# Optimization experiments

Hardware: AMD Instinct MI355X
Metric: run time of the kernel (lower is better)

Reference implementation:

```python
import jax, jax.numpy as jnp
import numpy as np

N, E, EQ, DIM = 50000, 800000, 100000, 256


def setup_inputs() -> dict:
    key = jax.random.key(0)
    k1, k2, k3, k4, k5 = jax.random.split(key, 5)
    edges = jax.random.randint(k1, (2, EQ), 0, N)
    adj_row = jax.random.randint(k2, (E,), 0, N)
    adj_col = jax.random.randint(k3, (E,), 0, N)
    node_weight = jax.random.uniform(k4, (N,), dtype=jnp.float32)
    # torchhd-style bipolar hypervectors scaled by sqrt(1/dim)
    scale = (1.0 / DIM) ** 0.5
    node_vectors = jnp.sign(jax.random.normal(k5, (N, DIM), dtype=jnp.float32)) * scale
    return dict(edges=edges, adj_row=adj_row, adj_col=adj_col,
                node_weight=node_weight, node_vectors=node_vectors)


def reference(edges, adj_row, adj_col, node_weight, node_vectors):
    n = node_vectors.shape[0]
    # get_random_node_vectors: embedding * node_weight
    x = node_vectors * node_weight[:, None]                       # [N, dim]
    # one_hop_x = A @ x ; two_hop_x = A @ one_hop_x (binary adjacency)
    one_hop = jax.ops.segment_sum(x[adj_col], adj_row, num_segments=n)       # [N, dim]
    two_hop = jax.ops.segment_sum(one_hop[adj_col], adj_row, num_segments=n)  # [N, dim]
    deg = jax.ops.segment_sum(jnp.ones(adj_row.shape, x.dtype), adj_row, num_segments=n)  # [N]
    s, t = edges[0], edges[1]
    dot = lambda a, b: (a * b).sum(-1)
    count_1_1 = dot(one_hop[s], one_hop[t])
    count_1_2 = dot(one_hop[s], two_hop[t]) + dot(two_hop[s], one_hop[t])
    count_2_2 = dot(two_hop[s] - deg[s][:, None] * x[s],
                    two_hop[t] - deg[t][:, None] * x[t])
    count_self_1_2 = dot(one_hop[s], two_hop[s]) + dot(one_hop[t], two_hop[t])
    return (count_1_1, count_1_2, count_2_2, count_self_1_2)
```

## Files before the change

### kernel.cpp

```cpp
#include <hip/hip_runtime.h>

#define DIM 256
#define NODE_U2 192
#define NODE_U4 96
#define SLOT_OH_U2 64
#define SLOT_TH_U2 128
#define SLOT_OH_U4 32
#define SLOT_TH_U4 64

#define NSL 8

__device__ __forceinline__ unsigned int f2bf_rne(float f) {
    unsigned int u = __float_as_uint(f);
    return (u + 0x7fffu + ((u >> 16) & 1u)) >> 16;
}
__device__ __forceinline__ float bf_lo(unsigned int u) {
    return __uint_as_float(u << 16);
}
__device__ __forceinline__ float bf_hi(unsigned int u) {
    return __uint_as_float(u & 0xffff0000u);
}
__device__ __forceinline__ unsigned int pack2(float a, float b) {
    return f2bf_rne(a) | (f2bf_rne(b) << 16);
}

#define ACC8(v)                                            \
    do {                                                   \
        a0 += bf_lo((v).x); a1 += bf_hi((v).x);            \
        a2 += bf_lo((v).y); a3 += bf_hi((v).y);            \
        a4 += bf_lo((v).z); a5 += bf_hi((v).z);            \
        a6 += bf_lo((v).w); a7 += bf_hi((v).w);            \
    } while (0)

__global__ void x_and_hist_kernel(const float* __restrict__ nv,
                                  const float* __restrict__ w,
                                  uint2* __restrict__ cmb,
                                  uint2* __restrict__ xs_sl,
                                  int total_u2, int N,
                                  const int* __restrict__ adj_row,
                                  int* __restrict__ cnt, int E) {
    int i0 = blockIdx.x * blockDim.x + threadIdx.x;
    int stride = gridDim.x * blockDim.x;
    for (int i = i0; i < total_u2; i += stride) {
        float4 v = reinterpret_cast<const float4*>(nv)[i];
        int node = i >> 6;
        int j = i & 63;
        float wt = w[node];
        uint2 r;
        r.x = pack2(v.x * wt, v.y * wt);
        r.y = pack2(v.z * wt, v.w * wt);
        cmb[(size_t)node * NODE_U2 + j] = r;
        int s = j >> 3;
        xs_sl[((size_t)s * N + node) * 8 + (j & 7)] = r;
    }
    for (int e = i0; e < E; e += stride) {
        atomicAdd(&cnt[adj_row[e]], 1);
    }
}

__global__ void block_sum_kernel(const int* __restrict__ in,
                                 int* __restrict__ sums, int n) {
    __shared__ int lds[256];
    int i = blockIdx.x * 256 + threadIdx.x;
    lds[threadIdx.x] = (i < n) ? in[i] : 0;
    __syncthreads();
    #pragma unroll
    for (int off = 128; off > 0; off >>= 1) {
        if (threadIdx.x < off) lds[threadIdx.x] += lds[threadIdx.x + off];
        __syncthreads();
    }
    if (threadIdx.x == 0) sums[blockIdx.x] = lds[0];
}

__global__ void scan_sums_kernel(int* __restrict__ sums, int nb,
                                 int* __restrict__ total_out) {
    __shared__ int lds[256];
    int v = (threadIdx.x < nb) ? sums[threadIdx.x] : 0;
    lds[threadIdx.x] = v;
    __syncthreads();
    #pragma unroll
    for (int off = 1; off < 256; off <<= 1) {
        int t = (threadIdx.x >= off) ? lds[threadIdx.x - off] : 0;
        __syncthreads();
        lds[threadIdx.x] += t;
        __syncthreads();
    }
    if (threadIdx.x < nb) sums[threadIdx.x] = lds[threadIdx.x] - v;
    if (threadIdx.x == 255) *total_out = lds[255];
}

__global__ void scan_block_kernel(const int* __restrict__ in,
                                  const int* __restrict__ sums,
                                  int* __restrict__ out1,
                                  int* __restrict__ out2, int n) {
    __shared__ int lds[256];
    int i = blockIdx.x * 256 + threadIdx.x;
    int v = (i < n) ? in[i] : 0;
    lds[threadIdx.x] = v;
    __syncthreads();
    #pragma unroll
    for (int off = 1; off < 256; off <<= 1) {
        int t = (threadIdx.x >= off) ? lds[threadIdx.x - off] : 0;
        __syncthreads();
        lds[threadIdx.x] += t;
        __syncthreads();
    }
    if (i < n) {
        int excl = sums[blockIdx.x] + lds[threadIdx.x] - v;
        out1[i] = excl;
        out2[i] = excl;
    }
}

__global__ void scatter_perm_kernel(const int* __restrict__ row,
                                    const int* __restrict__ col,
                                    int* __restrict__ cursor,
                                    int* __restrict__ perm, int nedges) {
    int e = blockIdx.x * blockDim.x + threadIdx.x;
    if (e < nedges) {
        int pos = atomicAdd(&cursor[row[e]], 1);
        perm[pos] = col[e];
    }
}

__global__ void gather_sliced_kernel(const int* __restrict__ row_ptr,
                                     const int* __restrict__ perm,
                                     const uint4* __restrict__ src_sl,
                                     uint4* __restrict__ dst_sl,
                                     uint4* __restrict__ dst_cmb_slot,
                                     int N) {
    int s = blockIdx.x & (NSL - 1);
    int rb = blockIdx.x >> 3;
    int g = threadIdx.x >> 2;
    int j = threadIdx.x & 3;
    int r = rb * 64 + g;
    if (r >= N) return;

    int beg = row_ptr[r];
    int end = row_ptr[r + 1];

    const uint4* base = src_sl + (size_t)s * N * 4;

    float a0 = 0.f, a1 = 0.f, a2 = 0.f, a3 = 0.f;
    float a4 = 0.f, a5 = 0.f, a6 = 0.f, a7 = 0.f;

    int e = beg;
    for (; e + 3 < end; e += 4) {
        int c0 = perm[e];
        int c1 = perm[e + 1];
        int c2 = perm[e + 2];
        int c3 = perm[e + 3];
        uint4 v0 = base[(size_t)c0 * 4 + j];
        uint4 v1 = base[(size_t)c1 * 4 + j];
        uint4 v2 = base[(size_t)c2 * 4 + j];
        uint4 v3 = base[(size_t)c3 * 4 + j];
        ACC8(v0); ACC8(v1); ACC8(v2); ACC8(v3);
    }
    for (; e < end; ++e) {
        int c = perm[e];
        uint4 v = base[(size_t)c * 4 + j];
        ACC8(v);
    }

    uint4 o;
    o.x = pack2(a0, a1);
    o.y = pack2(a2, a3);
    o.z = pack2(a4, a5);
    o.w = pack2(a6, a7);
    if (dst_sl) dst_sl[((size_t)s * N + r) * 4 + j] = o;
    dst_cmb_slot[(size_t)r * NODE_U4 + s * 4 + j] = o;
}

__global__ void query_kernel(const int* __restrict__ es,
                             const int* __restrict__ et,
                             const uint4* __restrict__ cmb4,
                             const int* __restrict__ row_ptr,
                             float* __restrict__ out, int nq) {
    int gid = blockIdx.x * blockDim.x + threadIdx.x;
    int q = gid >> 5;
    if (q >= nq) return;
    int l = gid & 31;

    int s = es[q];
    int t = et[q];

    const uint4* ns = cmb4 + (size_t)s * NODE_U4;
    const uint4* nt = cmb4 + (size_t)t * NODE_U4;

    uint4 vxs = ns[l];
    uint4 vos = ns[SLOT_OH_U4 + l];
    uint4 vts = ns[SLOT_TH_U4 + l];
    uint4 vxt = nt[l];
    uint4 vot = nt[SLOT_OH_U4 + l];
    uint4 vtt = nt[SLOT_TH_U4 + l];
    float ds = (float)(row_ptr[s + 1] - row_ptr[s]);
    float dt = (float)(row_ptr[t + 1] - row_ptr[t]);

    float c11 = 0.f, c12 = 0.f, c22 = 0.f, cs = 0.f;
    const unsigned int* pxs = (const unsigned int*)&vxs;
    const unsigned int* pxt = (const unsigned int*)&vxt;
    const unsigned int* pos_ = (const unsigned int*)&vos;
    const unsigned int* pot = (const unsigned int*)&vot;
    const unsigned int* pts = (const unsigned int*)&vts;
    const unsigned int* ptt = (const unsigned int*)&vtt;
    #pragma unroll
    for (int k = 0; k < 4; ++k) {
        {
            float fxs = bf_lo(pxs[k]), fxt = bf_lo(pxt[k]);
            float fos = bf_lo(pos_[k]), fot = bf_lo(pot[k]);
            float fts = bf_lo(pts[k]), ftt = bf_lo(ptt[k]);
            c11 += fos * fot;
            c12 += fos * ftt + fts * fot;
            float as = fts - ds * fxs;
            float bt = ftt - dt * fxt;
            c22 += as * bt;
            cs  += fos * fts + fot * ftt;
        }
        {
            float fxs = bf_hi(pxs[k]), fxt = bf_hi(pxt[k]);
            float fos = bf_hi(pos_[k]), fot = bf_hi(pot[k]);
            float fts = bf_hi(pts[k]), ftt = bf_hi(ptt[k]);
            c11 += fos * fot;
            c12 += fos * ftt + fts * fot;
            float as = fts - ds * fxs;
            float bt = ftt - dt * fxt;
            c22 += as * bt;
            cs  += fos * fts + fot * ftt;
        }
    }

    #pragma unroll
    for (int off = 16; off > 0; off >>= 1) {
        c11 += __shfl_xor(c11, off);
        c12 += __shfl_xor(c12, off);
        c22 += __shfl_xor(c22, off);
        cs  += __shfl_xor(cs,  off);
    }

    if (l == 0) {
        out[q]          = c11;
        out[nq + q]     = c12;
        out[2 * nq + q] = c22;
        out[3 * nq + q] = cs;
    }
}

extern "C" void kernel_launch(void* const* d_in, const int* in_sizes, int n_in,
                              void* d_out, int out_size, void* d_ws, size_t ws_size,
                              hipStream_t stream) {
    const int*   edges        = (const int*)  d_in[0];
    const int*   adj_row      = (const int*)  d_in[1];
    const int*   adj_col      = (const int*)  d_in[2];
    const float* node_weight  = (const float*)d_in[3];
    const float* node_vectors = (const float*)d_in[4];

    const int EQ = in_sizes[0] / 2;
    const int E  = in_sizes[1];
    const int N  = in_sizes[3];

    uint2* cmb   = (uint2*)d_ws;
    uint2* xs_sl = cmb + (size_t)N * NODE_U2;
    uint2* oh_sl = xs_sl + (size_t)N * NSL * 8;
    int* row_ptr = (int*)(oh_sl + (size_t)N * NSL * 8);
    int* cursor  = row_ptr + (N + 1);
    int* cnt     = cursor + N;
    int* perm    = cnt + N;
    int* s1      = perm + E;

    const int* es = edges;
    const int* et = edges + EQ;
    float* out = (float*)d_out;

    const int nb0 = (N + 255) / 256;

    hipMemsetAsync(cnt, 0, (size_t)N * sizeof(int), stream);
    int total_u2 = N * 64;
    x_and_hist_kernel<<<2048, 256, 0, stream>>>(node_vectors, node_weight,
                                                cmb, xs_sl, total_u2, N,
                                                adj_row, cnt, E);

    block_sum_kernel<<<nb0, 256, 0, stream>>>(cnt, s1, N);
    scan_sums_kernel<<<1, 256, 0, stream>>>(s1, nb0, row_ptr + N);
    scan_block_kernel<<<nb0, 256, 0, stream>>>(cnt, s1, row_ptr, cursor, N);
    scatter_perm_kernel<<<(E + 255) / 256, 256, 0, stream>>>(adj_row, adj_col,
                                                             cursor, perm, E);

    const uint4* xs4 = (const uint4*)xs_sl;
    uint4* oh4 = (uint4*)oh_sl;
    uint4* cmb4 = (uint4*)cmb;
    int nrb = (N + 63) / 64;
    int gblocks = nrb * NSL;
    gather_sliced_kernel<<<gblocks, 256, 0, stream>>>(
        row_ptr, perm, xs4, oh4, cmb4 + SLOT_OH_U4, N);
    gather_sliced_kernel<<<gblocks, 256, 0, stream>>>(
        row_ptr, perm, (const uint4*)oh4, (uint4*)nullptr,
        cmb4 + SLOT_TH_U4, N);

    int qthreads = EQ * 32;
    query_kernel<<<(qthreads + 255) / 256, 256, 0, stream>>>(
        es, et, cmb4, row_ptr, out, EQ);
}
```

Before: 256.4 us.

## Partition atomic histogram/scatter by row range and stage edge indices in LDS

Histogram and scatter kernels now assign each block one of 8 row-range partitions and read adj_row as int4. Each block issues atomics only for rows in its own range, so atomic traffic lands in a narrower address region per block, which is meant to improve L2 locality. The cost is that every block rereads the full row array, which is 8x more reads of it. The gather kernel preloads the block's contiguous perm slice into shared memory, up to 2048 entries, before the per-row gathers, with a global-memory fallback when a slice is larger.

```diff
diff --git a/kernel.cpp b/kernel.cpp
--- a/kernel.cpp
+++ b/kernel.cpp
@@ -3,12 +3,11 @@
 #define DIM 256
 #define NODE_U2 192
 #define NODE_U4 96
-#define SLOT_OH_U2 64
-#define SLOT_TH_U2 128
 #define SLOT_OH_U4 32
 #define SLOT_TH_U4 64
 
 #define NSL 8
+#define ECAP 2048
 
 __device__ __forceinline__ unsigned int f2bf_rne(float f) {
     unsigned int u = __float_as_uint(f);
@@ -38,7 +37,7 @@
                                   uint2* __restrict__ xs_sl,
                                   int total_u2, int N,
                                   const int* __restrict__ adj_row,
-                                  int* __restrict__ cnt, int E) {
+                                  int* __restrict__ cnt, int E, int per_part) {
     int i0 = blockIdx.x * blockDim.x + threadIdx.x;
     int stride = gridDim.x * blockDim.x;
     for (int i = i0; i < total_u2; i += stride) {
@@ -53,8 +52,21 @@
         int s = j >> 3;
         xs_sl[((size_t)s * N + node) * 8 + (j & 7)] = r;
     }
-    for (int e = i0; e < E; e += stride) {
-        atomicAdd(&cnt[adj_row[e]], 1);
+    int bp = blockIdx.x & 7;
+    unsigned lo = (unsigned)(bp * per_part);
+    int chunk = blockIdx.x >> 3;
+    int nchunks = gridDim.x >> 3;
+    int E4 = E >> 2;
+    for (int i = chunk * 256 + threadIdx.x; i < E4; i += nchunks * 256) {
+        int4 r4 = reinterpret_cast<const int4*>(adj_row)[i];
+        if ((unsigned)(r4.x - lo) < (unsigned)per_part) atomicAdd(&cnt[r4.x], 1);
+        if ((unsigned)(r4.y - lo) < (unsigned)per_part) atomicAdd(&cnt[r4.y], 1);
+        if ((unsigned)(r4.z - lo) < (unsigned)per_part) atomicAdd(&cnt[r4.z], 1);
+        if ((unsigned)(r4.w - lo) < (unsigned)per_part) atomicAdd(&cnt[r4.w], 1);
+    }
+    if (bp == 0 && chunk == 0) {
+        for (int e = (E & ~3) + threadIdx.x; e < E; e += 256)
+            atomicAdd(&cnt[adj_row[e]], 1);
     }
 }
 
@@ -112,14 +124,41 @@
     }
 }
 
-__global__ void scatter_perm_kernel(const int* __restrict__ row,
-                                    const int* __restrict__ col,
-                                    int* __restrict__ cursor,
-                                    int* __restrict__ perm, int nedges) {
-    int e = blockIdx.x * blockDim.x + threadIdx.x;
-    if (e < nedges) {
-        int pos = atomicAdd(&cursor[row[e]], 1);
-        perm[pos] = col[e];
+__global__ void scatter_perm_part_kernel(const int* __restrict__ row,
+                                         const int* __restrict__ col,
+                                         int* __restrict__ cursor,
+                                         int* __restrict__ perm,
+                                         int E, int per_part) {
+    int bp = blockIdx.x & 7;
+    unsigned lo = (unsigned)(bp * per_part);
+    int chunk = blockIdx.x >> 3;
+    int nchunks = gridDim.x >> 3;
+    int E4 = E >> 2;
+    for (int i = chunk * 256 + threadIdx.x; i < E4; i += nchunks * 256) {
+        int4 r4 = reinterpret_cast<const int4*>(row)[i];
+        int e = i << 2;
+        if ((unsigned)(r4.x - lo) < (unsigned)per_part) {
+            int pos = atomicAdd(&cursor[r4.x], 1);
+            perm[pos] = col[e];
+        }
+        if ((unsigned)(r4.y - lo) < (unsigned)per_part) {
+            int pos = atomicAdd(&cursor[r4.y], 1);
+            perm[pos] = col[e + 1];
+        }
+        if ((unsigned)(r4.z - lo) < (unsigned)per_part) {
+            int pos = atomicAdd(&cursor[r4.z], 1);
+            perm[pos] = col[e + 2];
+        }
+        if ((unsigned)(r4.w - lo) < (unsigned)per_part) {
+            int pos = atomicAdd(&cursor[r4.w], 1);
+            perm[pos] = col[e + 3];
+        }
+    }
+    if (bp == 0 && chunk == 0) {
+        for (int e = (E & ~3) + threadIdx.x; e < E; e += 256) {
+            int pos = atomicAdd(&cursor[row[e]], 1);
+            perm[pos] = col[e];
+        }
     }
 }
 
@@ -129,46 +168,63 @@
                                      uint4* __restrict__ dst_sl,
                                      uint4* __restrict__ dst_cmb_slot,
                                      int N) {
+    __shared__ int eidx[ECAP];
     int s = blockIdx.x & (NSL - 1);
     int rb = blockIdx.x >> 3;
+    int r0 = rb * 64;
+    int rlim = r0 + 64 < N ? r0 + 64 : N;
+    int beg0 = row_ptr[r0];
+    int end0 = row_ptr[rlim];
+    int L = end0 - beg0;
+    int Lc = L < ECAP ? L : ECAP;
+    for (int i = threadIdx.x; i < Lc; i += 256) eidx[i] = perm[beg0 + i];
+    __syncthreads();
+
     int g = threadIdx.x >> 2;
     int j = threadIdx.x & 3;
-    int r = rb * 64 + g;
+    int r = r0 + g;
     if (r >= N) return;
 
     int beg = row_ptr[r];
     int end = row_ptr[r + 1];
-
     const uint4* base = src_sl + (size_t)s * N * 4;
 
     float a0 = 0.f, a1 = 0.f, a2 = 0.f, a3 = 0.f;
     float a4 = 0.f, a5 = 0.f, a6 = 0.f, a7 = 0.f;
 
-    int e = beg;
-    for (; e + 3 < end; e += 4) {
-        int c0 = perm[e];
-        int c1 = perm[e + 1];
-        int c2 = perm[e + 2];
-        int c3 = perm[e + 3];
-        uint4 v0 = base[(size_t)c0 * 4 + j];
-        uint4 v1 = base[(size_t)c1 * 4 + j];
-        uint4 v2 = base[(size_t)c2 * 4 + j];
-        uint4 v3 = base[(size_t)c3 * 4 + j];
-        ACC8(v0); ACC8(v1); ACC8(v2); ACC8(v3);
-    }
-    for (; e < end; ++e) {
-        int c = perm[e];
-        uint4 v = base[(size_t)c * 4 + j];
-        ACC8(v);
-    }
-
-    uint4 o;
-    o.x = pack2(a0, a1);
-    o.y = pack2(a2, a3);
-    o.z = pack2(a4, a5);
-    o.w = pack2(a6, a7);
-    if (dst_sl) dst_sl[((size_t)s * N + r) * 4 + j] = o;
-    dst_cmb_slot[(size_t)r * NODE_U4 + s * 4 + j] = o;
+    if (end - beg0 <= ECAP) {
+        int o = beg - beg0;
+        int cnt = end - beg;
+        int k = 0;
+        for (; k + 3 < cnt; k += 4) {
+            int c0 = eidx[o + k];
+            int c1 = eidx[o + k + 1];
+            int c2 = eidx[o + k + 2];
+            int c3 = eidx[o + k + 3];
+            uint4 v0 = base[(size_t)c0 * 4 + j];
+            uint4 v1 = base[(size_t)c1 * 4 + j];
+            uint4 v2 = base[(size_t)c2 * 4 + j];
+            uint4 v3 = base[(size_t)c3 * 4 + j];
+            ACC8(v0); ACC8(v1); ACC8(v2); ACC8(v3);
+        }
+        for (; k < cnt; ++k) {
+            uint4 v = base[(size_t)eidx[o + k] * 4 + j];
+            ACC8(v);
+        }
+    } else {
+        for (int e = beg; e < end; ++e) {
+            uint4 v = base[(size_t)perm[e] * 4 + j];
+            ACC8(v);
+        }
+    }
+
+    uint4 o4;
+    o4.x = pack2(a0, a1);
+    o4.y = pack2(a2, a3);
+    o4.z = pack2(a4, a5);
+    o4.w = pack2(a6, a7);
+    if (dst_sl) dst_sl[((size_t)s * N + r) * 4 + j] = o4;
+    dst_cmb_slot[(size_t)r * NODE_U4 + s * 4 + j] = o4;
 }
 
 __global__ void query_kernel(const int* __restrict__ es,
@@ -272,18 +328,20 @@
     float* out = (float*)d_out;
 
     const int nb0 = (N + 255) / 256;
+    const int per_part = (N + 7) / 8;
 
     hipMemsetAsync(cnt, 0, (size_t)N * sizeof(int), stream);
     int total_u2 = N * 64;
     x_and_hist_kernel<<<2048, 256, 0, stream>>>(node_vectors, node_weight,
                                                 cmb, xs_sl, total_u2, N,
-                                                adj_row, cnt, E);
+                                                adj_row, cnt, E, per_part);
 
     block_sum_kernel<<<nb0, 256, 0, stream>>>(cnt, s1, N);
     scan_sums_kernel<<<1, 256, 0, stream>>>(s1, nb0, row_ptr + N);
     scan_block_kernel<<<nb0, 256, 0, stream>>>(cnt, s1, row_ptr, cursor, N);
-    scatter_perm_kernel<<<(E + 255) / 256, 256, 0, stream>>>(adj_row, adj_col,
-                                                             cursor, perm, E);
+    scatter_perm_part_kernel<<<2048, 256, 0, stream>>>(adj_row, adj_col,
+                                                       cursor, perm, E,
+                                                       per_part);
 
     const uint4* xs4 = (const uint4*)xs_sl;
     uint4* oh4 = (uint4*)oh_sl;
```

Result: faster. 232.4 us (-9.3%).
